# Optimization experiments

Measured on AMD Instinct MI355X. Metric: run time of the kernel, lower is better.

## Reference

```python
import jax, jax.numpy as jnp
import numpy as np

OUT = 7            # output_size
SR = 2             # sampling_ratio
SCALES = (0.25, 0.125, 0.0625, 0.03125)   # FPN strides 4,8,16,32
K_MIN, K_MAX = 2, 5
CANON_SCALE = 224.0
CANON_LVL = 4.0
EPS = 1e-6


def setup_inputs() -> dict:
    key = jax.random.key(0)
    ks = jax.random.split(key, 7)
    feat0 = jax.random.normal(ks[0], (2, 256, 200, 200), dtype=jnp.float32)
    feat1 = jax.random.normal(ks[1], (2, 256, 100, 100), dtype=jnp.float32)
    feat2 = jax.random.normal(ks[2], (2, 256, 50, 50), dtype=jnp.float32)
    feat3 = jax.random.normal(ks[3], (2, 256, 25, 25), dtype=jnp.float32)
    # boxes in 800x800 image coords: x1,y1 in [0,600), w,h in [2,200)
    xy = jax.random.uniform(ks[4], (2, 512, 2), dtype=jnp.float32) * 600.0
    wh = jax.random.uniform(ks[5], (2, 512, 2), dtype=jnp.float32) * 198.0 + 2.0
    boxes = jnp.concatenate([xy, xy + wh], axis=-1)  # [B,K,4] x1,y1,x2,y2
    return {"feat0": feat0, "feat1": feat1, "feat2": feat2, "feat3": feat3, "boxes": boxes}


def _bilinear(feat, bidx, ys, xs):
    # feat [B,C,H,W], bidx [N] int, ys [N,OY], xs [N,OX] -> [N,C,OY,OX]
    H, W = feat.shape[2], feat.shape[3]
    vy = (ys >= -1.0) & (ys <= float(H))
    vx = (xs >= -1.0) & (xs <= float(W))
    y = jnp.clip(ys, 0.0, H - 1.0)
    x = jnp.clip(xs, 0.0, W - 1.0)
    y0 = jnp.floor(y).astype(jnp.int32)
    x0 = jnp.floor(x).astype(jnp.int32)
    y1 = jnp.minimum(y0 + 1, H - 1)
    x1 = jnp.minimum(x0 + 1, W - 1)
    ly = y - y0
    lx = x - x0

    def g(yi, xi):
        # advanced indexing -> [N,OY,OX,C]
        return feat[bidx[:, None, None], :, yi[:, :, None], xi[:, None, :]]

    wy0 = (1.0 - ly)[:, :, None, None]
    wy1 = ly[:, :, None, None]
    wx0 = (1.0 - lx)[:, None, :, None]
    wx1 = lx[:, None, :, None]
    v = (wy0 * (wx0 * g(y0, x0) + wx1 * g(y0, x1))
         + wy1 * (wx0 * g(y1, x0) + wx1 * g(y1, x1)))
    v = v * (vy[:, :, None] & vx[:, None, :])[..., None].astype(v.dtype)
    return jnp.transpose(v, (0, 3, 1, 2))  # [N,C,OY,OX]


def _roi_align(feat, bidx, boxes, scale):
    # torchvision roi_align, aligned=False
    x1 = boxes[:, 0] * scale
    y1 = boxes[:, 1] * scale
    x2 = boxes[:, 2] * scale
    y2 = boxes[:, 3] * scale
    rw = jnp.maximum(x2 - x1, 1.0)
    rh = jnp.maximum(y2 - y1, 1.0)
    bw = rw / OUT
    bh = rh / OUT
    # flattened sample offsets: (j + 0.5)/SR in bin units, j in [0, OUT*SR)
    off = (jnp.arange(OUT * SR, dtype=jnp.float32) + 0.5) / SR
    ys = y1[:, None] + off[None, :] * bh[:, None]   # [N, OUT*SR]
    xs = x1[:, None] + off[None, :] * bw[:, None]   # [N, OUT*SR]
    v = _bilinear(feat, bidx, ys, xs)               # [N,C,OUT*SR,OUT*SR]
    N, C = v.shape[0], v.shape[1]
    v = v.reshape(N, C, OUT, SR, OUT, SR)
    return v.mean(axis=(3, 5))                      # [N,C,OUT,OUT]


def reference(feat0, feat1, feat2, feat3, boxes):
    feats = [feat0, feat1, feat2, feat3]
    B, K = boxes.shape[0], boxes.shape[1]
    boxes_f = boxes.reshape(-1, 4)                   # [N,4]
    bidx = jnp.repeat(jnp.arange(B, dtype=jnp.int32), K)
    # FPN level assignment (torchvision LevelMapper)
    area = (boxes_f[:, 2] - boxes_f[:, 0]) * (boxes_f[:, 3] - boxes_f[:, 1])
    lvl = jnp.floor(CANON_LVL + jnp.log2(jnp.sqrt(area) / CANON_SCALE + EPS))
    lvl = jnp.clip(lvl, K_MIN, K_MAX)
    idx = (lvl - K_MIN).astype(jnp.int32)            # [N] in {0..3}
    # compute ROI align at every level, select per box (jit-friendly)
    out = _roi_align(feats[0], bidx, boxes_f, SCALES[0])
    for l in range(1, 4):
        vl = _roi_align(feats[l], bidx, boxes_f, SCALES[l])
        out = jnp.where((idx == l)[:, None, None, None], vl, out)
    return out  # [B*K, C, 7, 7]
```

## Files before the change

### kernel.cpp

```cpp
#include <hip/hip_runtime.h>
#include <math.h>


constexpr int CH = 256;
constexpr int POUT = 7;
constexpr int NSAMP = 14;
constexpr int NBIN = POUT * POUT;
constexpr int PER_ROI = CH * NBIN;
constexpr int NWAVE = 2;
constexpr int CPW = 8;
constexpr int CPB = NWAVE * CPW;
constexpr int NCG = CH / CPB;

struct F2 { float x, y; };
__device__ inline F2 ld2(const float* p) {
    F2 v;
    __builtin_memcpy(&v, p, 8);
    return v;
}

__global__ __launch_bounds__(128)
void roi_align_sample_kernel(const float* __restrict__ f0,
                             const float* __restrict__ f1,
                             const float* __restrict__ f2,
                             const float* __restrict__ f3,
                             const float* __restrict__ boxes,
                             float* __restrict__ out,
                             int K)
{
    __shared__ alignas(16) float s_samp[NWAVE][256];
    __shared__ int   s_yr0[NSAMP], s_yr1[NSAMP];
    __shared__ float s_wy0[NSAMP], s_wy1[NSAMP];
    __shared__ int   s_xlc[NSAMP];
    __shared__ float s_ex0[NSAMP], s_ex1[NSAMP];

    const int tid  = threadIdx.x;
    const int wave = tid >> 6;
    const int lane = tid & 63;
    const int roi  = blockIdx.x >> 4;
    const int cg   = blockIdx.x & (NCG - 1);
    const int b    = roi / K;

    const float bx1 = boxes[roi * 4 + 0], by1 = boxes[roi * 4 + 1];
    const float bx2 = boxes[roi * 4 + 2], by2 = boxes[roi * 4 + 3];

    const float area = (bx2 - bx1) * (by2 - by1);
    float lvlf = floorf(4.0f + log2f(sqrtf(area) / 224.0f + 1e-6f));
    lvlf = fminf(fmaxf(lvlf, 2.0f), 5.0f);
    const int lvl = (int)lvlf - 2;

    const float* feat; int H, W; float scale;
    if (lvl == 0)      { feat = f0; H = 200; W = 200; scale = 0.25f;    }
    else if (lvl == 1) { feat = f1; H = 100; W = 100; scale = 0.125f;   }
    else if (lvl == 2) { feat = f2; H = 50;  W = 50;  scale = 0.0625f;  }
    else               { feat = f3; H = 25;  W = 25;  scale = 0.03125f; }

    const float x1 = bx1 * scale, y1 = by1 * scale;
    const float rw = fmaxf(bx2 * scale - x1, 1.0f);
    const float rh = fmaxf(by2 * scale - y1, 1.0f);
    const float bw = rw * (1.0f / POUT);
    const float bh = rh * (1.0f / POUT);

    if (tid < 2 * NSAMP) {
        const bool isY = tid < NSAMP;
        const int i = isY ? tid : tid - NSAMP;
        const float dim   = isY ? (float)H : (float)W;
        const float start = isY ? y1 : x1;
        const float bsz   = isY ? bh : bw;
        const float p = start + ((float)i + 0.5f) * 0.5f * bsz;
        const float valid = (p >= -1.0f && p <= dim) ? 1.0f : 0.0f;
        const float pc = fminf(fmaxf(p, 0.0f), dim - 1.0f);
        const int q0 = (int)floorf(pc);
        const float l = pc - (float)q0;
        const float w0 = (1.0f - l) * valid;
        const float w1 = l * valid;
        if (isY) {
            const int q1 = min(q0 + 1, (int)dim - 1);
            s_yr0[i] = q0 * W;
            s_yr1[i] = q1 * W;
            s_wy0[i] = w0;
            s_wy1[i] = w1;
        } else {
            const bool edge = (q0 > W - 2);
            s_xlc[i] = edge ? (W - 2) : q0;
            s_ex0[i] = edge ? 0.0f : w0;
            s_ex1[i] = edge ? (w1 + w0) : w1;
        }
    }
    __syncthreads();

    const int  ly   = lane / 14;
    const int  sx0  = lane - 14 * ly;
    const bool lact = (lane < 56);
    const int  sxc  = lact ? sx0 : 0;
    const int  xoff = s_xlc[sxc];
    const float e0  = s_ex0[sxc], e1 = s_ex1[sxc];

    int   offA[4], offB[4], wb[4];
    float wy0q[4], wy1q[4];
    bool  act[4];
    #pragma unroll
    for (int q = 0; q < 4; ++q) {
        const int  sy = 4 * q + ly;
        const bool a  = lact && (sy < NSAMP);
        act[q] = a;
        const int syc = a ? sy : 0;
        offA[q] = s_yr0[syc] + xoff;
        offB[q] = s_yr1[syc] + xoff;
        wy0q[q] = s_wy0[syc];
        wy1q[q] = s_wy1[syc];
        wb[q]   = 4 * ((sy >> 1) * POUT + (sxc >> 1)) + 2 * (sy & 1) + (sxc & 1);
    }

    const int HW = H * W;
    const int cbase = cg * CPB + wave * CPW;
    const float* chan0 = feat + ((size_t)b * CH + cbase) * (size_t)HW;
    float* sw = s_samp[wave];
    const size_t obase = (size_t)roi * PER_ROI + (size_t)cbase * NBIN + lane;

    F2 cA[4], cB[4], nA[4], nB[4];
    #pragma unroll
    for (int q = 0; q < 4; ++q) {
        cA[q] = ld2(chan0 + offA[q]);
        cB[q] = ld2(chan0 + offB[q]);
    }

    #pragma unroll
    for (int c = 0; c < CPW; ++c) {
        if (c + 1 < CPW) {
            const float* ch = chan0 + (size_t)(c + 1) * HW;
            #pragma unroll
            for (int q = 0; q < 4; ++q) {
                nA[q] = ld2(ch + offA[q]);
                nB[q] = ld2(ch + offB[q]);
            }
        }

        #pragma unroll
        for (int q = 0; q < 4; ++q) {
            const float sv = wy0q[q] * (e0 * cA[q].x + e1 * cA[q].y)
                           + wy1q[q] * (e0 * cB[q].x + e1 * cB[q].y);
            if (act[q]) sw[wb[q]] = sv;
        }

        asm volatile("s_waitcnt lgkmcnt(0)" ::: "memory");
        __builtin_amdgcn_sched_barrier(0);

        const float4 v = *(const float4*)(sw + 4 * lane);
        const float o = (v.x + v.y + v.z + v.w) * 0.25f;
        if (lane < NBIN) out[obase + (size_t)c * NBIN] = o;

        #pragma unroll
        for (int q = 0; q < 4; ++q) { cA[q] = nA[q]; cB[q] = nB[q]; }
    }
}

extern "C" void kernel_launch(void* const* d_in, const int* in_sizes, int n_in,
                              void* d_out, int out_size, void* d_ws, size_t ws_size,
                              hipStream_t stream) {
    const float* f0    = (const float*)d_in[0];
    const float* f1    = (const float*)d_in[1];
    const float* f2    = (const float*)d_in[2];
    const float* f3    = (const float*)d_in[3];
    const float* boxes = (const float*)d_in[4];
    float* out = (float*)d_out;

    const int B    = in_sizes[0] / (256 * 200 * 200);
    const int nroi = in_sizes[4] / 4;
    const int K    = nroi / B;

    roi_align_sample_kernel<<<nroi * NCG, 128, 0, stream>>>(f0, f1, f2, f3, boxes, out, K);
}
```

Before: 69.78 us.

## Stage narrow ROI windows into LDS via global_load_lds with double buffering

Splits the kernel into two template instantiations. The narrow one handles ROIs whose sampled columns fit in a 32-column window: it copies a 28x32 patch per channel into LDS with 16-byte global_load_lds, double-buffers across channels, and computes each output bin directly from LDS using XOR-swizzled indexes. The other ROIs use the original path. Both kernels launch over the full grid and return early when an ROI belongs to the other path, which adds a second launch and many empty blocks in exchange for wider, more coalesced loads.

```diff
diff --git a/kernel.cpp b/kernel.cpp
--- a/kernel.cpp
+++ b/kernel.cpp
@@ -7,10 +7,16 @@
 constexpr int NSAMP = 14;
 constexpr int NBIN = POUT * POUT;
 constexpr int PER_ROI = CH * NBIN;
+constexpr int SROWS = 28;
+constexpr int SCOLS = 32;
+constexpr int CHBUF = 1024;
 constexpr int NWAVE = 2;
 constexpr int CPW = 8;
 constexpr int CPB = NWAVE * CPW;
 constexpr int NCG = CH / CPB;
+
+#define ASG __attribute__((address_space(1)))
+#define ASL __attribute__((address_space(3)))
 
 struct F2 { float x, y; };
 __device__ inline F2 ld2(const float* p) {
@@ -19,18 +25,18 @@
     return v;
 }
 
+template <bool NARROW>
 __global__ __launch_bounds__(128)
-void roi_align_sample_kernel(const float* __restrict__ f0,
-                             const float* __restrict__ f1,
-                             const float* __restrict__ f2,
-                             const float* __restrict__ f3,
-                             const float* __restrict__ boxes,
-                             float* __restrict__ out,
-                             int K)
+void roi_kernel(const float* __restrict__ f0, const float* __restrict__ f1,
+                const float* __restrict__ f2, const float* __restrict__ f3,
+                const float* __restrict__ boxes, float* __restrict__ out, int K)
 {
-    __shared__ alignas(16) float s_samp[NWAVE][256];
-    __shared__ int   s_yr0[NSAMP], s_yr1[NSAMP];
+    constexpr int STAGEF = NARROW ? (NWAVE * 2 * CHBUF) : (NWAVE * 256);
+    __shared__ alignas(16) float s_stage[STAGEF];
+    __shared__ int   s_rowoff[SROWS];
     __shared__ float s_wy0[NSAMP], s_wy1[NSAMP];
+    __shared__ int2  s_xrel[NSAMP];
+    __shared__ float s_wx0[NSAMP], s_wx1[NSAMP];
     __shared__ int   s_xlc[NSAMP];
     __shared__ float s_ex0[NSAMP], s_ex1[NSAMP];
 
@@ -60,6 +66,14 @@
     const float rh = fmaxf(by2 * scale - y1, 1.0f);
     const float bw = rw * (1.0f / POUT);
     const float bh = rh * (1.0f / POUT);
+
+    const float pc0f  = fminf(fmaxf(x1 + (0.5f * 0.5f) * bw, 0.0f), (float)(W - 1));
+    const int   c0    = (int)floorf(pc0f);
+    const int   c0a   = c0 & ~3;
+    const float pc13f = fminf(fmaxf(x1 + (13.5f * 0.5f) * bw, 0.0f), (float)(W - 1));
+    const int   q13   = min((int)floorf(pc13f) + 1, W - 1);
+    const bool  isNarrow = ((W & 3) == 0) && (q13 - c0a <= SCOLS - 1);
+    if (isNarrow != NARROW) return;
 
     if (tid < 2 * NSAMP) {
         const bool isY = tid < NSAMP;
@@ -76,11 +90,16 @@
         const float w1 = l * valid;
         if (isY) {
             const int q1 = min(q0 + 1, (int)dim - 1);
-            s_yr0[i] = q0 * W;
-            s_yr1[i] = q1 * W;
+            s_rowoff[2 * i]     = q0 * W;
+            s_rowoff[2 * i + 1] = q1 * W;
             s_wy0[i] = w0;
             s_wy1[i] = w1;
         } else {
+            const int q1 = min(q0 + 1, (int)dim - 1);
+            s_xrel[i] = make_int2(min(max(q0 - c0a, 0), 63),
+                                  min(max(q1 - c0a, 0), 63));
+            s_wx0[i] = w0;
+            s_wx1[i] = w1;
             const bool edge = (q0 > W - 2);
             s_xlc[i] = edge ? (W - 2) : q0;
             s_ex0[i] = edge ? 0.0f : w0;
@@ -89,69 +108,149 @@
     }
     __syncthreads();
 
-    const int  ly   = lane / 14;
-    const int  sx0  = lane - 14 * ly;
-    const bool lact = (lane < 56);
-    const int  sxc  = lact ? sx0 : 0;
-    const int  xoff = s_xlc[sxc];
-    const float e0  = s_ex0[sxc], e1 = s_ex1[sxc];
-
-    int   offA[4], offB[4], wb[4];
-    float wy0q[4], wy1q[4];
-    bool  act[4];
-    #pragma unroll
-    for (int q = 0; q < 4; ++q) {
-        const int  sy = 4 * q + ly;
-        const bool a  = lact && (sy < NSAMP);
-        act[q] = a;
-        const int syc = a ? sy : 0;
-        offA[q] = s_yr0[syc] + xoff;
-        offB[q] = s_yr1[syc] + xoff;
-        wy0q[q] = s_wy0[syc];
-        wy1q[q] = s_wy1[syc];
-        wb[q]   = 4 * ((sy >> 1) * POUT + (sxc >> 1)) + 2 * (sy & 1) + (sxc & 1);
-    }
-
     const int HW = H * W;
     const int cbase = cg * CPB + wave * CPW;
     const float* chan0 = feat + ((size_t)b * CH + cbase) * (size_t)HW;
-    float* sw = s_samp[wave];
-    const size_t obase = (size_t)roi * PER_ROI + (size_t)cbase * NBIN + lane;
-
-    F2 cA[4], cB[4], nA[4], nB[4];
-    #pragma unroll
-    for (int q = 0; q < 4; ++q) {
-        cA[q] = ld2(chan0 + offA[q]);
-        cB[q] = ld2(chan0 + offB[q]);
-    }
-
-    #pragma unroll
-    for (int c = 0; c < CPW; ++c) {
-        if (c + 1 < CPW) {
-            const float* ch = chan0 + (size_t)(c + 1) * HW;
+
+    if constexpr (NARROW) {
+        const int lp = (lane < NBIN) ? lane : (NBIN - 1);
+        const int ph = lp / POUT, pw = lp - ph * POUT;
+        const int2  xra = s_xrel[2 * pw], xrb = s_xrel[2 * pw + 1];
+        const float wxa0 = s_wx0[2 * pw], wxa1 = s_wx1[2 * pw];
+        const float wxb0 = s_wx0[2 * pw + 1], wxb1 = s_wx1[2 * pw + 1];
+        const float wyA0 = s_wy0[2 * ph], wyA1 = s_wy1[2 * ph];
+        const float wyB0 = s_wy0[2 * ph + 1], wyB1 = s_wy1[2 * ph + 1];
+
+        const int sa0 = 4 * ((xra.x >> 2) ^ ph) + (xra.x & 3);
+        const int sa1 = 4 * ((xra.y >> 2) ^ ph) + (xra.y & 3);
+        const int sb0 = 4 * ((xrb.x >> 2) ^ ph) + (xrb.x & 3);
+        const int sb1 = 4 * ((xrb.y >> 2) ^ ph) + (xrb.y & 3);
+        const int rbase = 4 * ph * SCOLS;
+
+        int sidx[4];
+        #pragma unroll
+        for (int k = 0; k < 4; ++k) {
+            const int s = 64 * k + lane;
+            const int row = min(s >> 3, SROWS - 1);
+            const int g = s & 7;
+            sidx[k] = min(s_rowoff[row] + c0a + 4 * (g ^ (row >> 2)), HW - 4);
+        }
+
+        float* wstage = &s_stage[wave * 2 * CHBUF];
+        const size_t obase = (size_t)roi * PER_ROI + (size_t)cbase * NBIN + lp;
+
+#define STAGE(BUF, Q) do {                                                     \
+    __builtin_amdgcn_sched_barrier(0);                                         \
+    const float* ch_ = chan0 + (size_t)(Q) * HW;                               \
+    ASL float* ld_ = (ASL float*)(wstage + (BUF) * CHBUF);                     \
+    __builtin_amdgcn_global_load_lds((const ASG void*)(ch_ + sidx[0]),         \
+                                     (ASL void*)(ld_ + 0 * 256), 16, 0, 0);    \
+    __builtin_amdgcn_global_load_lds((const ASG void*)(ch_ + sidx[1]),         \
+                                     (ASL void*)(ld_ + 1 * 256), 16, 0, 0);    \
+    __builtin_amdgcn_global_load_lds((const ASG void*)(ch_ + sidx[2]),         \
+                                     (ASL void*)(ld_ + 2 * 256), 16, 0, 0);    \
+    __builtin_amdgcn_global_load_lds((const ASG void*)(ch_ + sidx[3]),         \
+                                     (ASL void*)(ld_ + 3 * 256), 16, 0, 0);    \
+} while (0)
+
+#define WAITV(N) do {                                                          \
+    asm volatile("s_waitcnt vmcnt(" #N ")" ::: "memory");                      \
+    __builtin_amdgcn_sched_barrier(0);                                         \
+} while (0)
+
+#define COMPUTE(BUF, Q) do {                                                   \
+    const float* rp_ = wstage + (BUF) * CHBUF + rbase;                         \
+    const float t00 = rp_[0 * SCOLS + sa0], t01 = rp_[0 * SCOLS + sa1];        \
+    const float t02 = rp_[0 * SCOLS + sb0], t03 = rp_[0 * SCOLS + sb1];        \
+    const float t10 = rp_[1 * SCOLS + sa0], t11 = rp_[1 * SCOLS + sa1];        \
+    const float t12 = rp_[1 * SCOLS + sb0], t13 = rp_[1 * SCOLS + sb1];        \
+    const float t20 = rp_[2 * SCOLS + sa0], t21 = rp_[2 * SCOLS + sa1];        \
+    const float t22 = rp_[2 * SCOLS + sb0], t23 = rp_[2 * SCOLS + sb1];        \
+    const float t30 = rp_[3 * SCOLS + sa0], t31 = rp_[3 * SCOLS + sa1];        \
+    const float t32 = rp_[3 * SCOLS + sb0], t33 = rp_[3 * SCOLS + sb1];        \
+    const float acc_ =                                                         \
+          wyA0 * (wxa0 * t00 + wxa1 * t01 + wxb0 * t02 + wxb1 * t03)           \
+        + wyA1 * (wxa0 * t10 + wxa1 * t11 + wxb0 * t12 + wxb1 * t13)           \
+        + wyB0 * (wxa0 * t20 + wxa1 * t21 + wxb0 * t22 + wxb1 * t23)           \
+        + wyB1 * (wxa0 * t30 + wxa1 * t31 + wxb0 * t32 + wxb1 * t33);          \
+    if (lane < NBIN) out[obase + (Q) * NBIN] = acc_ * 0.25f;                   \
+} while (0)
+
+        STAGE(0, 0);
+        STAGE(1, 1);
+        WAITV(4); COMPUTE(0, 0); STAGE(0, 2);
+        WAITV(4); COMPUTE(1, 1); STAGE(1, 3);
+        WAITV(4); COMPUTE(0, 2); STAGE(0, 4);
+        WAITV(4); COMPUTE(1, 3); STAGE(1, 5);
+        WAITV(4); COMPUTE(0, 4); STAGE(0, 6);
+        WAITV(4); COMPUTE(1, 5); STAGE(1, 7);
+        WAITV(4); COMPUTE(0, 6);
+        WAITV(0); COMPUTE(1, 7);
+#undef STAGE
+#undef WAITV
+#undef COMPUTE
+    } else {
+        const int  ly   = lane / 14;
+        const int  sx0  = lane - 14 * ly;
+        const bool lact = (lane < 56);
+        const int  sxc  = lact ? sx0 : 0;
+        const int  xoff = s_xlc[sxc];
+        const float e0  = s_ex0[sxc], e1 = s_ex1[sxc];
+
+        int   offA[4], offB[4], wb[4];
+        float wy0q[4], wy1q[4];
+        bool  act[4];
+        #pragma unroll
+        for (int q = 0; q < 4; ++q) {
+            const int  sy = 4 * q + ly;
+            const bool a  = lact && (sy < NSAMP);
+            act[q] = a;
+            const int syc = a ? sy : 0;
+            offA[q] = s_rowoff[2 * syc]     + xoff;
+            offB[q] = s_rowoff[2 * syc + 1] + xoff;
+            wy0q[q] = s_wy0[syc];
+            wy1q[q] = s_wy1[syc];
+            wb[q]   = 4 * ((sy >> 1) * POUT + (sxc >> 1)) + 2 * (sy & 1) + (sxc & 1);
+        }
+
+        float* sw = &s_stage[wave * 256];
+        const size_t obase = (size_t)roi * PER_ROI + (size_t)cbase * NBIN + lane;
+
+        F2 cA[4], cB[4], nA[4], nB[4];
+        #pragma unroll
+        for (int q = 0; q < 4; ++q) {
+            cA[q] = ld2(chan0 + offA[q]);
+            cB[q] = ld2(chan0 + offB[q]);
+        }
+
+        #pragma unroll
+        for (int c = 0; c < CPW; ++c) {
+            if (c + 1 < CPW) {
+                const float* ch = chan0 + (size_t)(c + 1) * HW;
+                #pragma unroll
+                for (int q = 0; q < 4; ++q) {
+                    nA[q] = ld2(ch + offA[q]);
+                    nB[q] = ld2(ch + offB[q]);
+                }
+            }
+
             #pragma unroll
             for (int q = 0; q < 4; ++q) {
-                nA[q] = ld2(ch + offA[q]);
-                nB[q] = ld2(ch + offB[q]);
+                const float sv = wy0q[q] * (e0 * cA[q].x + e1 * cA[q].y)
+                               + wy1q[q] * (e0 * cB[q].x + e1 * cB[q].y);
+                if (act[q]) sw[wb[q]] = sv;
             }
-        }
-
-        #pragma unroll
-        for (int q = 0; q < 4; ++q) {
-            const float sv = wy0q[q] * (e0 * cA[q].x + e1 * cA[q].y)
-                           + wy1q[q] * (e0 * cB[q].x + e1 * cB[q].y);
-            if (act[q]) sw[wb[q]] = sv;
-        }
-
-        asm volatile("s_waitcnt lgkmcnt(0)" ::: "memory");
-        __builtin_amdgcn_sched_barrier(0);
-
-        const float4 v = *(const float4*)(sw + 4 * lane);
-        const float o = (v.x + v.y + v.z + v.w) * 0.25f;
-        if (lane < NBIN) out[obase + (size_t)c * NBIN] = o;
-
-        #pragma unroll
-        for (int q = 0; q < 4; ++q) { cA[q] = nA[q]; cB[q] = nB[q]; }
+
+            asm volatile("s_waitcnt lgkmcnt(0)" ::: "memory");
+            __builtin_amdgcn_sched_barrier(0);
+
+            const float4 v = *(const float4*)(sw + 4 * lane);
+            const float o = (v.x + v.y + v.z + v.w) * 0.25f;
+            if (lane < NBIN) out[obase + (size_t)c * NBIN] = o;
+
+            #pragma unroll
+            for (int q = 0; q < 4; ++q) { cA[q] = nA[q]; cB[q] = nB[q]; }
+        }
     }
 }
 
@@ -169,5 +268,6 @@
     const int nroi = in_sizes[4] / 4;
     const int K    = nroi / B;
 
-    roi_align_sample_kernel<<<nroi * NCG, 128, 0, stream>>>(f0, f1, f2, f3, boxes, out, K);
+    roi_kernel<true><<<nroi * NCG, 128, 0, stream>>>(f0, f1, f2, f3, boxes, out, K);
+    roi_kernel<false><<<nroi * NCG, 128, 0, stream>>>(f0, f1, f2, f3, boxes, out, K);
 }
```

After: 76.42 us. 1.1x slower.

## Compute each output bin per lane, drop LDS reduction, use float4 row loads

Applied to the files above, without the earlier changes.

Work is remapped so each lane owns one output bin and accumulates its four sample points in registers. This removes the shared-memory scratch write, the LDS wait and the float4 readback used to average samples. When the two x-samples of every bin fall within four columns, each row is fetched with a single 16-byte load and precombined weights. Otherwise the kernel falls back to 8-byte pair loads. The cost is fewer active lanes (49 of 64) and unaligned 16-byte loads, with a uniform branch on box width.

```diff
diff --git a/kernel.cpp b/kernel.cpp
--- a/kernel.cpp
+++ b/kernel.cpp
@@ -13,23 +13,20 @@
 constexpr int NCG = CH / CPB;
 
 struct F2 { float x, y; };
-__device__ inline F2 ld2(const float* p) {
-    F2 v;
-    __builtin_memcpy(&v, p, 8);
-    return v;
-}
+__device__ inline F2 ld2(const float* p) { F2 v; __builtin_memcpy(&v, p, 8); return v; }
+struct F4 { float x, y, z, w; };
+__device__ inline F4 ld4(const float* p) { F4 v; __builtin_memcpy(&v, p, 16); return v; }
 
 __global__ __launch_bounds__(128)
-void roi_align_sample_kernel(const float* __restrict__ f0,
-                             const float* __restrict__ f1,
-                             const float* __restrict__ f2,
-                             const float* __restrict__ f3,
-                             const float* __restrict__ boxes,
-                             float* __restrict__ out,
-                             int K)
+void roi_align_bin_kernel(const float* __restrict__ f0,
+                          const float* __restrict__ f1,
+                          const float* __restrict__ f2,
+                          const float* __restrict__ f3,
+                          const float* __restrict__ boxes,
+                          float* __restrict__ out,
+                          int K)
 {
-    __shared__ alignas(16) float s_samp[NWAVE][256];
-    __shared__ int   s_yr0[NSAMP], s_yr1[NSAMP];
+    __shared__ int   s_rowoff[2 * NSAMP];
     __shared__ float s_wy0[NSAMP], s_wy1[NSAMP];
     __shared__ int   s_xlc[NSAMP];
     __shared__ float s_ex0[NSAMP], s_ex1[NSAMP];
@@ -76,8 +73,8 @@
         const float w1 = l * valid;
         if (isY) {
             const int q1 = min(q0 + 1, (int)dim - 1);
-            s_yr0[i] = q0 * W;
-            s_yr1[i] = q1 * W;
+            s_rowoff[2 * i]     = q0 * W;
+            s_rowoff[2 * i + 1] = q1 * W;
             s_wy0[i] = w0;
             s_wy1[i] = w1;
         } else {
@@ -89,69 +86,90 @@
     }
     __syncthreads();
 
-    const int  ly   = lane / 14;
-    const int  sx0  = lane - 14 * ly;
-    const bool lact = (lane < 56);
-    const int  sxc  = lact ? sx0 : 0;
-    const int  xoff = s_xlc[sxc];
-    const float e0  = s_ex0[sxc], e1 = s_ex1[sxc];
+    bool narrow = true;
+    #pragma unroll
+    for (int j = 0; j < POUT; ++j)
+        narrow = narrow && (s_xlc[2 * j + 1] - s_xlc[2 * j] <= 2);
 
-    int   offA[4], offB[4], wb[4];
-    float wy0q[4], wy1q[4];
-    bool  act[4];
-    #pragma unroll
-    for (int q = 0; q < 4; ++q) {
-        const int  sy = 4 * q + ly;
-        const bool a  = lact && (sy < NSAMP);
-        act[q] = a;
-        const int syc = a ? sy : 0;
-        offA[q] = s_yr0[syc] + xoff;
-        offB[q] = s_yr1[syc] + xoff;
-        wy0q[q] = s_wy0[syc];
-        wy1q[q] = s_wy1[syc];
-        wb[q]   = 4 * ((sy >> 1) * POUT + (sxc >> 1)) + 2 * (sy & 1) + (sxc & 1);
-    }
+    const int  lp = (lane < NBIN) ? lane : (NBIN - 1);
+    const bool act = (lane < NBIN);
+    const int  by = lp / POUT, bx = lp - POUT * by;
+
+    const int ro0 = s_rowoff[4 * by + 0];
+    const int ro1 = s_rowoff[4 * by + 1];
+    const int ro2 = s_rowoff[4 * by + 2];
+    const int ro3 = s_rowoff[4 * by + 3];
+    const float wy0 = s_wy0[2 * by],     wy1 = s_wy1[2 * by];
+    const float wy2 = s_wy0[2 * by + 1], wy3 = s_wy1[2 * by + 1];
+
+    const int lc0 = s_xlc[2 * bx], lc1 = s_xlc[2 * bx + 1];
+    const float e00 = s_ex0[2 * bx],     e01 = s_ex1[2 * bx];
+    const float e10 = s_ex0[2 * bx + 1], e11 = s_ex1[2 * bx + 1];
 
     const int HW = H * W;
     const int cbase = cg * CPB + wave * CPW;
     const float* chan0 = feat + ((size_t)b * CH + cbase) * (size_t)HW;
-    float* sw = s_samp[wave];
-    const size_t obase = (size_t)roi * PER_ROI + (size_t)cbase * NBIN + lane;
+    const size_t obase = (size_t)roi * PER_ROI + (size_t)cbase * NBIN + lp;
 
-    F2 cA[4], cB[4], nA[4], nB[4];
-    #pragma unroll
-    for (int q = 0; q < 4; ++q) {
-        cA[q] = ld2(chan0 + offA[q]);
-        cB[q] = ld2(chan0 + offB[q]);
-    }
+    if (narrow) {
+        const int base = min(lc0, W - 4);
+        const int i0 = lc0 - base;
+        const int i1 = lc1 - base;
+        const float w40 = (i0 == 0 ? e00 : 0.0f) + (i1 == 0 ? e10 : 0.0f);
+        const float w41 = (i0 == 1 ? e00 : 0.0f) + (i0 == 0 ? e01 : 0.0f)
+                        + (i1 == 1 ? e10 : 0.0f) + (i1 == 0 ? e11 : 0.0f);
+        const float w42 = (i0 == 2 ? e00 : 0.0f) + (i0 == 1 ? e01 : 0.0f)
+                        + (i1 == 2 ? e10 : 0.0f) + (i1 == 1 ? e11 : 0.0f);
+        const float w43 = (i0 == 2 ? e01 : 0.0f) + (i1 == 2 ? e11 : 0.0f);
 
-    #pragma unroll
-    for (int c = 0; c < CPW; ++c) {
-        if (c + 1 < CPW) {
-            const float* ch = chan0 + (size_t)(c + 1) * HW;
-            #pragma unroll
-            for (int q = 0; q < 4; ++q) {
-                nA[q] = ld2(ch + offA[q]);
-                nB[q] = ld2(ch + offB[q]);
-            }
-        }
+        F4 v0 = ld4(chan0 + ro0 + base);
+        F4 v1 = ld4(chan0 + ro1 + base);
+        F4 v2 = ld4(chan0 + ro2 + base);
+        F4 v3 = ld4(chan0 + ro3 + base);
 
         #pragma unroll
-        for (int q = 0; q < 4; ++q) {
-            const float sv = wy0q[q] * (e0 * cA[q].x + e1 * cA[q].y)
-                           + wy1q[q] * (e0 * cB[q].x + e1 * cB[q].y);
-            if (act[q]) sw[wb[q]] = sv;
+        for (int c = 0; c < CPW; ++c) {
+            F4 n0, n1, n2, n3;
+            if (c + 1 < CPW) {
+                const float* ch = chan0 + (size_t)(c + 1) * HW;
+                n0 = ld4(ch + ro0 + base);
+                n1 = ld4(ch + ro1 + base);
+                n2 = ld4(ch + ro2 + base);
+                n3 = ld4(ch + ro3 + base);
+            }
+            const float rv0 = v0.x * w40 + v0.y * w41 + v0.z * w42 + v0.w * w43;
+            const float rv1 = v1.x * w40 + v1.y * w41 + v1.z * w42 + v1.w * w43;
+            const float rv2 = v2.x * w40 + v2.y * w41 + v2.z * w42 + v2.w * w43;
+            const float rv3 = v3.x * w40 + v3.y * w41 + v3.z * w42 + v3.w * w43;
+            const float acc = wy0 * rv0 + wy1 * rv1 + wy2 * rv2 + wy3 * rv3;
+            if (act) out[obase + (size_t)c * NBIN] = acc * 0.25f;
+            v0 = n0; v1 = n1; v2 = n2; v3 = n3;
         }
-
-        asm volatile("s_waitcnt lgkmcnt(0)" ::: "memory");
-        __builtin_amdgcn_sched_barrier(0);
-
-        const float4 v = *(const float4*)(sw + 4 * lane);
-        const float o = (v.x + v.y + v.z + v.w) * 0.25f;
-        if (lane < NBIN) out[obase + (size_t)c * NBIN] = o;
+    } else {
+        F2 a0 = ld2(chan0 + ro0 + lc0), d0 = ld2(chan0 + ro0 + lc1);
+        F2 a1 = ld2(chan0 + ro1 + lc0), d1 = ld2(chan0 + ro1 + lc1);
+        F2 a2 = ld2(chan0 + ro2 + lc0), d2 = ld2(chan0 + ro2 + lc1);
+        F2 a3 = ld2(chan0 + ro3 + lc0), d3 = ld2(chan0 + ro3 + lc1);
 
         #pragma unroll
-        for (int q = 0; q < 4; ++q) { cA[q] = nA[q]; cB[q] = nB[q]; }
+        for (int c = 0; c < CPW; ++c) {
+            F2 na0, na1, na2, na3, nd0, nd1, nd2, nd3;
+            if (c + 1 < CPW) {
+                const float* ch = chan0 + (size_t)(c + 1) * HW;
+                na0 = ld2(ch + ro0 + lc0); nd0 = ld2(ch + ro0 + lc1);
+                na1 = ld2(ch + ro1 + lc0); nd1 = ld2(ch + ro1 + lc1);
+                na2 = ld2(ch + ro2 + lc0); nd2 = ld2(ch + ro2 + lc1);
+                na3 = ld2(ch + ro3 + lc0); nd3 = ld2(ch + ro3 + lc1);
+            }
+            const float rv0 = e00 * a0.x + e01 * a0.y + e10 * d0.x + e11 * d0.y;
+            const float rv1 = e00 * a1.x + e01 * a1.y + e10 * d1.x + e11 * d1.y;
+            const float rv2 = e00 * a2.x + e01 * a2.y + e10 * d2.x + e11 * d2.y;
+            const float rv3 = e00 * a3.x + e01 * a3.y + e10 * d3.x + e11 * d3.y;
+            const float acc = wy0 * rv0 + wy1 * rv1 + wy2 * rv2 + wy3 * rv3;
+            if (act) out[obase + (size_t)c * NBIN] = acc * 0.25f;
+            a0 = na0; a1 = na1; a2 = na2; a3 = na3;
+            d0 = nd0; d1 = nd1; d2 = nd2; d3 = nd3;
+        }
     }
 }
 
@@ -169,5 +187,5 @@
     const int nroi = in_sizes[4] / 4;
     const int K    = nroi / B;
 
-    roi_align_sample_kernel<<<nroi * NCG, 128, 0, stream>>>(f0, f1, f2, f3, boxes, out, K);
+    roi_align_bin_kernel<<<nroi * NCG, 128, 0, stream>>>(f0, f1, f2, f3, boxes, out, K);
 }
```

Measured after the change: 64.06 us (median of 2 runs). 1.09x faster.
